# Performance work log

Measured on AMD Instinct MI355X. Metric: run time of the kernel, lower is better.

## Reference

```python
import jax, jax.numpy as jnp
import numpy as np

T, B, IN, H, OUT, L = 2048, 16, 72, 256, 90, 2


def setup_inputs() -> dict:
    key = jax.random.key(0)
    ks = jax.random.split(key, 12)
    s = 0.05
    x = jax.random.normal(ks[0], (T, B, IN), jnp.float32)
    lengths = jnp.clip(jax.random.randint(ks[1], (B,), 1, T + 1), 1, T)
    W1 = jax.random.normal(ks[2], (H, IN), jnp.float32) * s
    b1 = jax.random.normal(ks[3], (H,), jnp.float32) * s
    Wih = jax.random.normal(ks[4], (L, 4 * H, H), jnp.float32) * s
    Whh = jax.random.normal(ks[5], (L, 4 * H, H), jnp.float32) * s
    bih = jax.random.normal(ks[6], (L, 4 * H), jnp.float32) * s
    bhh = jax.random.normal(ks[7], (L, 4 * H), jnp.float32) * s
    W2 = jax.random.normal(ks[8], (OUT, H), jnp.float32) * s
    b2 = jax.random.normal(ks[9], (OUT,), jnp.float32) * s
    return dict(x=x, lengths=lengths, W1=W1, b1=b1, Wih=Wih, Whh=Whh,
                bih=bih, bhh=bhh, W2=W2, b2=b2)


def _lstm_layer(x, mask, Wih, Whh, bih, bhh):
    # x: [T,B,H], mask: [T,B] bool (True = valid frame)
    Hh = Whh.shape[1]
    Bsz = x.shape[1]
    # input projection for all timesteps at once (the only big GEMM)
    gi = jnp.einsum('tbi,gi->tbg', x, Wih) + bih  # [T,B,4H]

    def step(carry, inp):
        h, c = carry
        g_in, m = inp
        g = g_in + h @ Whh.T + bhh
        i, f, gg, o = jnp.split(g, 4, axis=-1)  # PyTorch gate order i,f,g,o
        c_new = jax.nn.sigmoid(f) * c + jax.nn.sigmoid(i) * jnp.tanh(gg)
        h_new = jax.nn.sigmoid(o) * jnp.tanh(c_new)
        m2 = m[:, None]
        # pack semantics: state frozen past each sequence's length, output zero
        h = jnp.where(m2, h_new, h)
        c = jnp.where(m2, c_new, c)
        return (h, c), jnp.where(m2, h_new, jnp.zeros_like(h_new))

    init = (jnp.zeros((Bsz, Hh), x.dtype), jnp.zeros((Bsz, Hh), x.dtype))
    _, ys = jax.lax.scan(step, init, (gi, mask))
    return ys


def reference(x, lengths, W1, b1, Wih, Whh, bih, bhh, W2, b2):
    # linear1 + relu (dropout=0 -> identity)
    h = jax.nn.relu(jnp.einsum('tbi,hi->tbh', x, W1) + b1)
    mask = jnp.arange(T)[:, None] < lengths[None, :]  # [T,B]
    for l in range(L):
        h = _lstm_layer(h, mask, Wih[l], Whh[l], bih[l], bhh[l])
    y = jnp.einsum('tbh,oh->tbo', h, W2) + b2
    # zero out padded frames (they are discarded by the per-sequence slicing)
    return jnp.where(mask[:, :, None], y, jnp.zeros_like(y))
```

## Files before the change

### kernel.cpp

```cpp
#include <hip/hip_runtime.h>
#include <hip/hip_bf16.h>

#define T_STEPS 2048
#define HID 256
#define INF 72
#define OUTF 90
#define HSTR 528

typedef __attribute__((ext_vector_type(4))) float f32x4;
typedef __attribute__((ext_vector_type(8))) short s16x8;

__device__ __forceinline__ unsigned short f2bf(float f) {
  union { float f; unsigned u; } v; v.f = f;
  unsigned r = (v.u + 0x7FFFu + ((v.u >> 16) & 1u)) >> 16;
  return (unsigned short)r;
}
__device__ __forceinline__ float bf2f(unsigned short s) {
  union { unsigned u; float f; } v; v.u = ((unsigned)s) << 16;
  return v.f;
}
__device__ __forceinline__ float sigm(float x) {
  return __builtin_amdgcn_rcpf(1.f + __builtin_amdgcn_exp2f(-1.44269504f * x));
}
__device__ __forceinline__ float tanh_f(float x) {
  return 1.f - 2.f * __builtin_amdgcn_rcpf(1.f + __builtin_amdgcn_exp2f(2.88539008f * x));
}

__global__ __launch_bounds__(256) void inproj(const float* __restrict__ x,
                                              const float* __restrict__ W1,
                                              const float* __restrict__ b1,
                                              float* __restrict__ h0) {
  __shared__ float w1s[HID][INF + 1];
  __shared__ float xs[16][INF];
  const int tid = threadIdx.x;
  const int r0 = blockIdx.x * 16;
  for (int i = tid; i < HID * INF; i += 256) w1s[i / INF][i % INF] = W1[i];
  for (int i = tid; i < 16 * INF; i += 256)
    xs[i / INF][i % INF] = x[(size_t)(r0 + i / INF) * INF + (i % INF)];
  __syncthreads();
  const float bj = b1[tid];
  for (int r = 0; r < 16; ++r) {
    float acc = bj;
#pragma unroll 8
    for (int k = 0; k < INF; ++k) acc += xs[r][k] * w1s[tid][k];
    h0[(size_t)(r0 + r) * HID + tid] = fmaxf(acc, 0.f);
  }
}

__global__ __launch_bounds__(256) void wpack(const float* __restrict__ w,
                                             unsigned short* __restrict__ o) {
  const size_t i = ((size_t)blockIdx.x * 256 + threadIdx.x) * 8;
  f32x4 a = *(const f32x4*)(w + i);
  f32x4 b = *(const f32x4*)(w + i + 4);
  s16x8 v;
#pragma unroll
  for (int e = 0; e < 4; ++e) { v[e] = (short)f2bf(a[e]); v[4 + e] = (short)f2bf(b[e]); }
  *(s16x8*)(o + i) = v;
}

__global__ __launch_bounds__(256) void gi_mfma(const float* __restrict__ h,
                                               const unsigned short* __restrict__ wb,
                                               const float* __restrict__ bih,
                                               const float* __restrict__ bhh,
                                               unsigned short* __restrict__ gi) {
  __shared__ __align__(16) char hs[16 * HSTR];
  __shared__ float bs[1024];
  const int tid = threadIdx.x;
  const int t = blockIdx.x;
  const int lane = tid & 63;
  const int wg = tid >> 6;
  const int j = lane & 15;
  const int hi = lane >> 4;
  for (int i = tid; i < 1024; i += 256) bs[i] = bih[i] + bhh[i];
  {
    const int row = tid >> 4;
    const int c0 = (tid & 15) * 16;
    const float* src = h + ((size_t)t * 16 + row) * 256 + c0;
    f32x4 v0 = *(const f32x4*)(src);
    f32x4 v1 = *(const f32x4*)(src + 4);
    f32x4 v2 = *(const f32x4*)(src + 8);
    f32x4 v3 = *(const f32x4*)(src + 12);
    s16x8 p0, p1;
#pragma unroll
    for (int e = 0; e < 4; ++e) {
      p0[e] = (short)f2bf(v0[e]); p0[4 + e] = (short)f2bf(v1[e]);
      p1[e] = (short)f2bf(v2[e]); p1[4 + e] = (short)f2bf(v3[e]);
    }
    *(s16x8*)(hs + row * HSTR + c0 * 2) = p0;
    *(s16x8*)(hs + row * HSTR + c0 * 2 + 16) = p1;
  }
  __syncthreads();
  const int hread = j * HSTR + hi * 16;
  f32x4 acc[4][4] = {};
#pragma unroll
  for (int kt = 0; kt < 8; ++kt) {
    const int k = kt * 32 + hi * 8;
    const s16x8 a = *(const s16x8*)(hs + hread + kt * 64);
#pragma unroll
    for (int ug2 = 0; ug2 < 4; ++ug2)
#pragma unroll
      for (int q = 0; q < 4; ++q) {
        const s16x8 b = *(const s16x8*)(wb + (((size_t)(q << 8) + wg * 64 + ug2 * 16 + j) << 8) + k);
        acc[ug2][q] = __builtin_amdgcn_mfma_f32_16x16x32_bf16(a, b, acc[ug2][q], 0, 0, 0);
      }
  }
#pragma unroll
  for (int ug2 = 0; ug2 < 4; ++ug2) {
    const int sw = wg * 4 + ug2;
    const int u0 = wg * 64 + ug2 * 16 + j;
    s16x8 o0, o1;
#pragma unroll
    for (int r = 0; r < 4; ++r) {
      o0[r]     = (short)f2bf(acc[ug2][0][r] + bs[u0]);
      o0[4 + r] = (short)f2bf(acc[ug2][1][r] + bs[256 + u0]);
      o1[r]     = (short)f2bf(acc[ug2][2][r] + bs[512 + u0]);
      o1[4 + r] = (short)f2bf(acc[ug2][3][r] + bs[768 + u0]);
    }
    unsigned short* dst = gi + ((size_t)(t * 16 + sw) * 64 + lane) * 16;
    *(s16x8*)(dst) = o0;
    *(s16x8*)(dst + 8) = o1;
  }
}


template <int ROLE>
__device__ __forceinline__ void scan2cu(
    const unsigned short* __restrict__ gi,
    const unsigned short* __restrict__ whbL,
    const int* __restrict__ lengths,
    unsigned short* __restrict__ hb1,
    float* __restrict__ hout,
    unsigned short* hx,
    unsigned* myflag, unsigned* peerflag,
    unsigned* cntA, unsigned* cntB,
    int half)
{
  const int tid  = threadIdx.x;
  const int lane = tid & 63;
  const int w    = tid >> 6;
  const int j    = lane & 15;
  const int hi   = lane >> 4;
  const int u    = half * 128 + w * 16 + j;

  s16x8 wfr[32];
#pragma unroll
  for (int kt = 0; kt < 8; ++kt)
#pragma unroll
    for (int q = 0; q < 4; ++q)
      wfr[kt * 4 + q] =
          *(const s16x8*)(whbL + ((size_t)(q * 256 + u) << 8) + kt * 32 + hi * 8);

  int len[4];
#pragma unroll
  for (int r = 0; r < 4; ++r) len[r] = lengths[hi * 4 + r];
  float c[4] = {};
  unsigned short hprev[4] = {};

  {
    unsigned* z = (unsigned*)hx;
    for (int i = tid; i < 1024; i += 512)
      z[(i >> 6) * 128 + half * 64 + (i & 63)] = 0u;
  }
  asm volatile("s_waitcnt vmcnt(0)" ::: "memory");
  __builtin_amdgcn_s_barrier();
  if (tid == 0) __hip_atomic_store(myflag, 1u, __ATOMIC_RELEASE, __HIP_MEMORY_SCOPE_AGENT);

  unsigned cred = 0;
  if (ROLE == 1) {
    while (cred < 8u) {
      unsigned a = __hip_atomic_load(cntA, __ATOMIC_ACQUIRE, __HIP_MEMORY_SCOPE_AGENT);
      unsigned b = __hip_atomic_load(cntB, __ATOMIC_ACQUIRE, __HIP_MEMORY_SCOPE_AGENT);
      cred = a < b ? a : b;
      if (cred < 8u) __builtin_amdgcn_s_sleep(2);
    }
  }
  const unsigned short* gp = gi + ((size_t)(half * 8 + w) * 64 + lane) * 16;
  s16x8 gE0 = *(const s16x8*)(gp);
  s16x8 gE1 = *(const s16x8*)(gp + 8);
  s16x8 gO0 = *(const s16x8*)(gp + 16384);
  s16x8 gO1 = *(const s16x8*)(gp + 16384 + 8);

  for (int tg = 0; tg < T_STEPS; tg += 4) {
    if (ROLE == 1) {
      const unsigned target = (tg + 8 <= T_STEPS) ? (unsigned)(tg + 8) : (unsigned)T_STEPS;
      while (cred < target) {
        unsigned a = __hip_atomic_load(cntA, __ATOMIC_ACQUIRE, __HIP_MEMORY_SCOPE_AGENT);
        unsigned b = __hip_atomic_load(cntB, __ATOMIC_ACQUIRE, __HIP_MEMORY_SCOPE_AGENT);
        cred = a < b ? a : b;
        if (cred < target) __builtin_amdgcn_s_sleep(2);
      }
    }
#pragma unroll
    for (int ts = 0; ts < 4; ++ts) {
      const int t = tg + ts;
      s16x8& g0 = (ts & 1) ? gO0 : gE0;
      s16x8& g1 = (ts & 1) ? gO1 : gE1;

      while (__hip_atomic_load(peerflag, __ATOMIC_ACQUIRE, __HIP_MEMORY_SCOPE_AGENT) < (unsigned)(t + 1))
        __builtin_amdgcn_s_sleep(1);

      const unsigned short* hsrc = hx + (size_t)(t & 3) * 4096 + j * 256 + hi * 8;
      s16x8 av[8];
#pragma unroll
      for (int kt = 0; kt < 8; ++kt) av[kt] = *(const s16x8*)(hsrc + kt * 32);

      f32x4 acc[4];
#pragma unroll
      for (int r = 0; r < 4; ++r) {
        acc[0][r] = bf2f((unsigned short)g0[r]);
        acc[1][r] = bf2f((unsigned short)g0[4 + r]);
        acc[2][r] = bf2f((unsigned short)g1[r]);
        acc[3][r] = bf2f((unsigned short)g1[4 + r]);
      }
      {
        const int tn = (t + 2 < T_STEPS) ? t + 2 : T_STEPS - 1;
        const unsigned short* gn = gp + (size_t)tn * 16384;
        g0 = *(const s16x8*)(gn);
        g1 = *(const s16x8*)(gn + 8);
      }
#pragma unroll
      for (int kt = 0; kt < 8; ++kt)
#pragma unroll
        for (int q = 0; q < 4; ++q)
          acc[q] = __builtin_amdgcn_mfma_f32_16x16x32_bf16(av[kt], wfr[kt * 4 + q], acc[q], 0, 0, 0);

      unsigned short* hdst = hx + (size_t)((t + 1) & 3) * 4096;
#pragma unroll
      for (int r = 0; r < 4; ++r) {
        const float i_  = sigm(acc[0][r]);
        const float f_  = sigm(acc[1][r]);
        const float tg_ = tanh_f(acc[2][r]);
        const float o_  = sigm(acc[3][r]);
        const float cn = f_ * c[r] + i_ * tg_;
        const float hv = o_ * tanh_f(cn);
        const bool m = t < len[r];
        c[r] = m ? cn : c[r];
        const unsigned short hb = m ? f2bf(hv) : hprev[r];
        hprev[r] = hb;
        const int b = hi * 4 + r;
        hdst[b * 256 + u] = hb;
        if (ROLE == 0) hb1[(size_t)t * 4096 + b * 256 + u] = m ? hb : (unsigned short)0;
        else           hout[((size_t)t * 16 + b) * 256 + u] = m ? hv : 0.f;
      }
      asm volatile("s_waitcnt vmcnt(0)" ::: "memory");
      __builtin_amdgcn_s_barrier();
      if (tid == 0)
        __hip_atomic_store(myflag, (unsigned)(t + 2), __ATOMIC_RELEASE, __HIP_MEMORY_SCOPE_AGENT);
      asm volatile("" ::: "memory");
    }
  }
}

__device__ __forceinline__ void gi2b(int qbase,
    const unsigned short* __restrict__ hb1,
    const unsigned short* __restrict__ wb2,
    const float* __restrict__ bih2, const float* __restrict__ bhh2,
    unsigned short* __restrict__ gf2,
    unsigned* f1a, unsigned* f1b, unsigned* cnt_out)
{
  const int tid = threadIdx.x;
  const int lane = tid & 63;
  const int w = tid >> 6;
  const int j = lane & 15;
  const int hi = lane >> 4;

  s16x8 wfr[2][2][8];
  float bsum[2][2];
#pragma unroll
  for (int qh = 0; qh < 2; ++qh)
#pragma unroll
    for (int ug = 0; ug < 2; ++ug) {
      const int col = (qbase + qh) * 256 + w * 32 + ug * 16 + j;
      bsum[qh][ug] = bih2[col] + bhh2[col];
#pragma unroll
      for (int kt = 0; kt < 8; ++kt)
        wfr[qh][ug][kt] = *(const s16x8*)(wb2 + ((size_t)col << 8) + kt * 32 + hi * 8);
    }

  const int qoff = qbase * 4;
  unsigned cred = 0;
  for (int tg = 0; tg < T_STEPS; tg += 4) {
    const unsigned target = (unsigned)(tg + 5);
    while (cred < target) {
      unsigned a = __hip_atomic_load(f1a, __ATOMIC_ACQUIRE, __HIP_MEMORY_SCOPE_AGENT);
      unsigned b = __hip_atomic_load(f1b, __ATOMIC_ACQUIRE, __HIP_MEMORY_SCOPE_AGENT);
      cred = a < b ? a : b;
      if (cred < target) __builtin_amdgcn_s_sleep(2);
    }
#pragma unroll
    for (int ts = 0; ts < 4; ++ts) {
      const int t = tg + ts;
      const unsigned short* ab = hb1 + (size_t)t * 4096 + j * 256 + hi * 8;
      f32x4 acc[2][2];
#pragma unroll
      for (int qh = 0; qh < 2; ++qh)
#pragma unroll
        for (int ug = 0; ug < 2; ++ug)
#pragma unroll
          for (int r = 0; r < 4; ++r) acc[qh][ug][r] = bsum[qh][ug];
#pragma unroll
      for (int kt = 0; kt < 8; ++kt) {
        const s16x8 a = *(const s16x8*)(ab + kt * 32);
#pragma unroll
        for (int qh = 0; qh < 2; ++qh)
#pragma unroll
          for (int ug = 0; ug < 2; ++ug)
            acc[qh][ug] = __builtin_amdgcn_mfma_f32_16x16x32_bf16(a, wfr[qh][ug][kt], acc[qh][ug], 0, 0, 0);
      }
#pragma unroll
      for (int ug = 0; ug < 2; ++ug) {
        s16x8 o;
#pragma unroll
        for (int r = 0; r < 4; ++r) {
          o[r]     = (short)f2bf(acc[0][ug][r]);
          o[4 + r] = (short)f2bf(acc[1][ug][r]);
        }
        *(s16x8*)(gf2 + ((size_t)(t * 16 + w * 2 + ug) * 64 + lane) * 16 + qoff) = o;
      }
    }
    asm volatile("s_waitcnt vmcnt(0)" ::: "memory");
    __builtin_amdgcn_s_barrier();
    if (tid == 0)
      __hip_atomic_store(cnt_out, (unsigned)(tg + 4), __ATOMIC_RELEASE, __HIP_MEMORY_SCOPE_AGENT);
    asm volatile("" ::: "memory");
  }
}

__global__ __launch_bounds__(512, 2) void fused_pipe(
    const unsigned short* __restrict__ gf1,
    const unsigned short* __restrict__ whb,
    const unsigned short* __restrict__ wb,
    const float* __restrict__ bih, const float* __restrict__ bhh,
    const int* __restrict__ lengths,
    unsigned short* hb1, unsigned short* gf2, float* hout2,
    unsigned short* hx1, unsigned short* hx2, unsigned* sync)
{
  const int bid = blockIdx.x;
  if (bid == 0)
    scan2cu<0>(gf1, whb, lengths, hb1, nullptr, hx1, sync + 0, sync + 32, nullptr, nullptr, 0);
  else if (bid == 8)
    scan2cu<0>(gf1, whb, lengths, hb1, nullptr, hx1, sync + 32, sync + 0, nullptr, nullptr, 1);
  else if (bid == 1)
    scan2cu<1>(gf2, whb + 262144, lengths, nullptr, hout2, hx2, sync + 64, sync + 96, sync + 128, sync + 160, 0);
  else if (bid == 9)
    scan2cu<1>(gf2, whb + 262144, lengths, nullptr, hout2, hx2, sync + 96, sync + 64, sync + 128, sync + 160, 1);
  else if (bid == 2)
    gi2b(0, hb1, wb + 262144, bih + 1024, bhh + 1024, gf2, sync + 0, sync + 32, sync + 128);
  else if (bid == 10)
    gi2b(2, hb1, wb + 262144, bih + 1024, bhh + 1024, gf2, sync + 0, sync + 32, sync + 160);
}

__global__ __launch_bounds__(256) void outproj(const float* __restrict__ h2,
                                               const float* __restrict__ W2,
                                               const float* __restrict__ b2,
                                               const int* __restrict__ lengths,
                                               float* __restrict__ y) {
  __shared__ float w2s[OUTF][HID + 1];
  __shared__ float hs[8][HID + 1];
  const int tid = threadIdx.x;
  const int r0 = blockIdx.x * 8;
  for (int i = tid; i < OUTF * HID; i += 256) w2s[i / HID][i % HID] = W2[i];
  for (int i = tid; i < 8 * HID; i += 256)
    hs[i / HID][i % HID] = h2[(size_t)(r0 + i / HID) * HID + (i % HID)];
  __syncthreads();
  for (int oi = tid; oi < 8 * OUTF; oi += 256) {
    const int r = oi / OUTF, o = oi % OUTF;
    const int row = r0 + r, t = row >> 4, b = row & 15;
    float acc = b2[o];
#pragma unroll 8
    for (int k = 0; k < HID; ++k) acc += hs[r][k] * w2s[o][k];
    y[(size_t)row * OUTF + o] = (t < lengths[b]) ? acc : 0.f;
  }
}

extern "C" void kernel_launch(void* const* d_in, const int* in_sizes, int n_in,
                              void* d_out, int out_size, void* d_ws, size_t ws_size,
                              hipStream_t stream) {
  const float* x      = (const float*)d_in[0];
  const int*   lengths= (const int*)d_in[1];
  const float* W1     = (const float*)d_in[2];
  const float* b1     = (const float*)d_in[3];
  const float* Wih    = (const float*)d_in[4];
  const float* Whh    = (const float*)d_in[5];
  const float* bih    = (const float*)d_in[6];
  const float* bhh    = (const float*)d_in[7];
  const float* W2     = (const float*)d_in[8];
  const float* b2     = (const float*)d_in[9];
  float* out = (float*)d_out;

  char* ws = (char*)d_ws;
  float*          h0   = (float*)(ws);
  unsigned short* gf1  = (unsigned short*)(ws + 33554432);
  unsigned short* hb1  = (unsigned short*)(ws + 100663296);
  unsigned short* gf2  = (unsigned short*)(ws + 117440512);
  float*          h2o  = (float*)(ws + 184549376);
  unsigned short* wb   = (unsigned short*)(ws + 218103808);
  unsigned short* whb  = (unsigned short*)(ws + 219152384);
  unsigned short* hx1  = (unsigned short*)(ws + 220200960);
  unsigned short* hx2  = (unsigned short*)(ws + 220233728);
  unsigned*       sync = (unsigned*)(ws + 220266496);

  wpack<<<256, 256, 0, stream>>>(Wih, wb);
  wpack<<<256, 256, 0, stream>>>(Whh, whb);
  inproj<<<2048, 256, 0, stream>>>(x, W1, b1, h0);
  gi_mfma<<<2048, 256, 0, stream>>>(h0, wb, bih, bhh, gf1);

  hipMemsetAsync((void*)sync, 0, 768, stream);
  fused_pipe<<<11, 512, 0, stream>>>(gf1, whb, wb, bih, bhh, lengths,
                                     hb1, gf2, h2o, hx1, hx2, sync);

  outproj<<<4096, 256, 0, stream>>>(h2o, W2, b2, lengths, out);
}
```

Measured before the change: 10.66 ms.

## Replace per-step block barriers with per-wave flags and transposed MFMA layout

The recurrent scan drops the workgroup barrier and single release flag per timestep. Instead each wave publishes its own relaxed flag, and consumers poll all 16 wave flags with 64-bit loads. The MFMA operands are swapped so each lane holds four consecutive hidden units of one batch. That lets h and outputs be written as packed 64-bit stores and lengths be read once per lane. The gi2b producer is reorganised to compute all four gates per wave. The goal is to cut barrier and cross-CU synchronisation latency on the serial critical path, relying on relaxed atomics plus vmcnt waits for ordering.

```diff
diff --git a/kernel.cpp b/kernel.cpp
--- a/kernel.cpp
+++ b/kernel.cpp
@@ -9,6 +9,7 @@
 
 typedef __attribute__((ext_vector_type(4))) float f32x4;
 typedef __attribute__((ext_vector_type(8))) short s16x8;
+typedef unsigned long long u64;
 
 __device__ __forceinline__ unsigned short f2bf(float f) {
   union { float f; unsigned u; } v; v.f = f;
@@ -24,6 +25,38 @@
 }
 __device__ __forceinline__ float tanh_f(float x) {
   return 1.f - 2.f * __builtin_amdgcn_rcpf(1.f + __builtin_amdgcn_exp2f(2.88539008f * x));
+}
+
+__device__ __forceinline__ u64 ld64(const u64* p) {
+  return __hip_atomic_load(p, __ATOMIC_RELAXED, __HIP_MEMORY_SCOPE_AGENT);
+}
+__device__ __forceinline__ void st64(u64* p, u64 v) {
+  __hip_atomic_store(p, v, __ATOMIC_RELAXED, __HIP_MEMORY_SCOPE_AGENT);
+}
+__device__ __forceinline__ void stflag(unsigned* p, unsigned v) {
+  __hip_atomic_store(p, v, __ATOMIC_RELAXED, __HIP_MEMORY_SCOPE_AGENT);
+}
+__device__ __forceinline__ void wait16(const unsigned* flags, unsigned target) {
+  const u64* fl = (const u64*)flags;
+  unsigned mn;
+  do {
+    mn = 0xFFFFFFFFu;
+#pragma unroll
+    for (int i = 0; i < 8; ++i) {
+      u64 v = ld64(fl + i);
+      unsigned a = (unsigned)v, b = (unsigned)(v >> 32);
+      mn = a < mn ? a : mn;
+      mn = b < mn ? b : mn;
+    }
+    if (mn < target) __builtin_amdgcn_s_sleep(1);
+  } while (mn < target);
+}
+__device__ __forceinline__ void ld_gi(const unsigned short* p, s16x8& a, s16x8& b) {
+  const u64* q = (const u64*)p;
+  union { u64 u[2]; s16x8 v; } x, y;
+  x.u[0] = ld64(q + 0); x.u[1] = ld64(q + 1);
+  y.u[0] = ld64(q + 2); y.u[1] = ld64(q + 3);
+  a = x.v; b = y.v;
 }
 
 __global__ __launch_bounds__(256) void inproj(const float* __restrict__ x,
@@ -100,21 +133,21 @@
     for (int ug2 = 0; ug2 < 4; ++ug2)
 #pragma unroll
       for (int q = 0; q < 4; ++q) {
-        const s16x8 b = *(const s16x8*)(wb + (((size_t)(q << 8) + wg * 64 + ug2 * 16 + j) << 8) + k);
-        acc[ug2][q] = __builtin_amdgcn_mfma_f32_16x16x32_bf16(a, b, acc[ug2][q], 0, 0, 0);
+        const s16x8 bw = *(const s16x8*)(wb + (((size_t)(q << 8) + wg * 64 + ug2 * 16 + j) << 8) + k);
+        acc[ug2][q] = __builtin_amdgcn_mfma_f32_16x16x32_bf16(bw, a, acc[ug2][q], 0, 0, 0);
       }
   }
 #pragma unroll
   for (int ug2 = 0; ug2 < 4; ++ug2) {
     const int sw = wg * 4 + ug2;
-    const int u0 = wg * 64 + ug2 * 16 + j;
+    const int uT = sw * 16 + hi * 4;
     s16x8 o0, o1;
 #pragma unroll
     for (int r = 0; r < 4; ++r) {
-      o0[r]     = (short)f2bf(acc[ug2][0][r] + bs[u0]);
-      o0[4 + r] = (short)f2bf(acc[ug2][1][r] + bs[256 + u0]);
-      o1[r]     = (short)f2bf(acc[ug2][2][r] + bs[512 + u0]);
-      o1[4 + r] = (short)f2bf(acc[ug2][3][r] + bs[768 + u0]);
+      o0[r]     = (short)f2bf(acc[ug2][0][r] + bs[uT + r]);
+      o0[4 + r] = (short)f2bf(acc[ug2][1][r] + bs[256 + uT + r]);
+      o1[r]     = (short)f2bf(acc[ug2][2][r] + bs[512 + uT + r]);
+      o1[4 + r] = (short)f2bf(acc[ug2][3][r] + bs[768 + uT + r]);
     }
     unsigned short* dst = gi + ((size_t)(t * 16 + sw) * 64 + lane) * 16;
     *(s16x8*)(dst) = o0;
@@ -131,8 +164,8 @@
     unsigned short* __restrict__ hb1,
     float* __restrict__ hout,
     unsigned short* hx,
-    unsigned* myflag, unsigned* peerflag,
-    unsigned* cntA, unsigned* cntB,
+    unsigned* flags,
+    unsigned* creds,
     int half)
 {
   const int tid  = threadIdx.x;
@@ -140,7 +173,8 @@
   const int w    = tid >> 6;
   const int j    = lane & 15;
   const int hi   = lane >> 4;
-  const int u    = half * 128 + w * 16 + j;
+  const int uB   = half * 128 + w * 16;
+  const int myf  = half * 8 + w;
 
   s16x8 wfr[32];
 #pragma unroll
@@ -148,44 +182,35 @@
 #pragma unroll
     for (int q = 0; q < 4; ++q)
       wfr[kt * 4 + q] =
-          *(const s16x8*)(whbL + ((size_t)(q * 256 + u) << 8) + kt * 32 + hi * 8);
-
-  int len[4];
-#pragma unroll
-  for (int r = 0; r < 4; ++r) len[r] = lengths[hi * 4 + r];
+          *(const s16x8*)(whbL + ((size_t)(q * 256 + uB + j) << 8) + kt * 32 + hi * 8);
+
+  const int len = lengths[j];
   float c[4] = {};
   unsigned short hprev[4] = {};
 
-  {
-    unsigned* z = (unsigned*)hx;
-    for (int i = tid; i < 1024; i += 512)
-      z[(i >> 6) * 128 + half * 64 + (i & 63)] = 0u;
-  }
-  asm volatile("s_waitcnt vmcnt(0)" ::: "memory");
-  __builtin_amdgcn_s_barrier();
-  if (tid == 0) __hip_atomic_store(myflag, 1u, __ATOMIC_RELEASE, __HIP_MEMORY_SCOPE_AGENT);
+  const unsigned short* gp = gi + ((size_t)(half * 8 + w) * 64 + lane) * 16;
 
   unsigned cred = 0;
   if (ROLE == 1) {
+    const u64* cp = (const u64*)creds;
     while (cred < 8u) {
-      unsigned a = __hip_atomic_load(cntA, __ATOMIC_ACQUIRE, __HIP_MEMORY_SCOPE_AGENT);
-      unsigned b = __hip_atomic_load(cntB, __ATOMIC_ACQUIRE, __HIP_MEMORY_SCOPE_AGENT);
+      u64 v = ld64(cp);
+      unsigned a = (unsigned)v, b = (unsigned)(v >> 32);
       cred = a < b ? a : b;
       if (cred < 8u) __builtin_amdgcn_s_sleep(2);
     }
   }
-  const unsigned short* gp = gi + ((size_t)(half * 8 + w) * 64 + lane) * 16;
-  s16x8 gE0 = *(const s16x8*)(gp);
-  s16x8 gE1 = *(const s16x8*)(gp + 8);
-  s16x8 gO0 = *(const s16x8*)(gp + 16384);
-  s16x8 gO1 = *(const s16x8*)(gp + 16384 + 8);
+  s16x8 gE0, gE1, gO0, gO1;
+  ld_gi(gp, gE0, gE1);
+  ld_gi(gp + 16384, gO0, gO1);
 
   for (int tg = 0; tg < T_STEPS; tg += 4) {
     if (ROLE == 1) {
       const unsigned target = (tg + 8 <= T_STEPS) ? (unsigned)(tg + 8) : (unsigned)T_STEPS;
+      const u64* cp = (const u64*)creds;
       while (cred < target) {
-        unsigned a = __hip_atomic_load(cntA, __ATOMIC_ACQUIRE, __HIP_MEMORY_SCOPE_AGENT);
-        unsigned b = __hip_atomic_load(cntB, __ATOMIC_ACQUIRE, __HIP_MEMORY_SCOPE_AGENT);
+        u64 v = ld64(cp);
+        unsigned a = (unsigned)v, b = (unsigned)(v >> 32);
         cred = a < b ? a : b;
         if (cred < target) __builtin_amdgcn_s_sleep(2);
       }
@@ -196,13 +221,17 @@
       s16x8& g0 = (ts & 1) ? gO0 : gE0;
       s16x8& g1 = (ts & 1) ? gO1 : gE1;
 
-      while (__hip_atomic_load(peerflag, __ATOMIC_ACQUIRE, __HIP_MEMORY_SCOPE_AGENT) < (unsigned)(t + 1))
-        __builtin_amdgcn_s_sleep(1);
-
-      const unsigned short* hsrc = hx + (size_t)(t & 3) * 4096 + j * 256 + hi * 8;
+      wait16(flags, (unsigned)t);
+
+      const u64* hsrc = (const u64*)(hx + (size_t)(t & 3) * 4096 + j * 256) + hi * 2;
       s16x8 av[8];
 #pragma unroll
-      for (int kt = 0; kt < 8; ++kt) av[kt] = *(const s16x8*)(hsrc + kt * 32);
+      for (int kt = 0; kt < 8; ++kt) {
+        union { u64 u[2]; s16x8 v; } x;
+        x.u[0] = ld64(hsrc + kt * 8);
+        x.u[1] = ld64(hsrc + kt * 8 + 1);
+        av[kt] = x.v;
+      }
 
       f32x4 acc[4];
 #pragma unroll
@@ -214,17 +243,17 @@
       }
       {
         const int tn = (t + 2 < T_STEPS) ? t + 2 : T_STEPS - 1;
-        const unsigned short* gn = gp + (size_t)tn * 16384;
-        g0 = *(const s16x8*)(gn);
-        g1 = *(const s16x8*)(gn + 8);
+        ld_gi(gp + (size_t)tn * 16384, g0, g1);
       }
 #pragma unroll
       for (int kt = 0; kt < 8; ++kt)
 #pragma unroll
         for (int q = 0; q < 4; ++q)
-          acc[q] = __builtin_amdgcn_mfma_f32_16x16x32_bf16(av[kt], wfr[kt * 4 + q], acc[q], 0, 0, 0);
-
-      unsigned short* hdst = hx + (size_t)((t + 1) & 3) * 4096;
+          acc[q] = __builtin_amdgcn_mfma_f32_16x16x32_bf16(wfr[kt * 4 + q], av[kt], acc[q], 0, 0, 0);
+
+      u64 hpk = 0, ypk = 0;
+      f32x4 yv;
+      const bool m = t < len;
 #pragma unroll
       for (int r = 0; r < 4; ++r) {
         const float i_  = sigm(acc[0][r]);
@@ -233,96 +262,96 @@
         const float o_  = sigm(acc[3][r]);
         const float cn = f_ * c[r] + i_ * tg_;
         const float hv = o_ * tanh_f(cn);
-        const bool m = t < len[r];
         c[r] = m ? cn : c[r];
         const unsigned short hb = m ? f2bf(hv) : hprev[r];
         hprev[r] = hb;
-        const int b = hi * 4 + r;
-        hdst[b * 256 + u] = hb;
-        if (ROLE == 0) hb1[(size_t)t * 4096 + b * 256 + u] = m ? hb : (unsigned short)0;
-        else           hout[((size_t)t * 16 + b) * 256 + u] = m ? hv : 0.f;
-      }
+        hpk |= (u64)hb << (16 * r);
+        if (ROLE == 0) ypk |= (u64)(m ? hb : (unsigned short)0) << (16 * r);
+        else           yv[r] = m ? hv : 0.f;
+      }
+      st64((u64*)hx + ((((t + 1) & 3) * 4096 + j * 256 + uB + hi * 4) >> 2), hpk);
+      if (ROLE == 0)
+        st64((u64*)hb1 + (((size_t)t * 4096 + j * 256 + uB + hi * 4) >> 2), ypk);
+      else
+        *(f32x4*)(hout + ((size_t)t * 16 + j) * 256 + uB + hi * 4) = yv;
       asm volatile("s_waitcnt vmcnt(0)" ::: "memory");
-      __builtin_amdgcn_s_barrier();
-      if (tid == 0)
-        __hip_atomic_store(myflag, (unsigned)(t + 2), __ATOMIC_RELEASE, __HIP_MEMORY_SCOPE_AGENT);
-      asm volatile("" ::: "memory");
-    }
-  }
-}
-
-__device__ __forceinline__ void gi2b(int qbase,
+      if (lane == 0) stflag(flags + myf, (unsigned)(t + 1));
+    }
+  }
+}
+
+__device__ __forceinline__ void gi2b(int cu,
     const unsigned short* __restrict__ hb1,
     const unsigned short* __restrict__ wb2,
     const float* __restrict__ bih2, const float* __restrict__ bhh2,
     unsigned short* __restrict__ gf2,
-    unsigned* f1a, unsigned* f1b, unsigned* cnt_out)
+    unsigned* flags1, unsigned* cred)
 {
   const int tid = threadIdx.x;
   const int lane = tid & 63;
   const int w = tid >> 6;
   const int j = lane & 15;
   const int hi = lane >> 4;
-
-  s16x8 wfr[2][2][8];
-  float bsum[2][2];
-#pragma unroll
-  for (int qh = 0; qh < 2; ++qh)
-#pragma unroll
-    for (int ug = 0; ug < 2; ++ug) {
-      const int col = (qbase + qh) * 256 + w * 32 + ug * 16 + j;
-      bsum[qh][ug] = bih2[col] + bhh2[col];
-#pragma unroll
-      for (int kt = 0; kt < 8; ++kt)
-        wfr[qh][ug][kt] = *(const s16x8*)(wb2 + ((size_t)col << 8) + kt * 32 + hi * 8);
-    }
-
-  const int qoff = qbase * 4;
-  unsigned cred = 0;
+  const int sw = cu * 8 + w;
+
+  s16x8 wfr[32];
+  float bsum[4][4];
+#pragma unroll
+  for (int kt = 0; kt < 8; ++kt)
+#pragma unroll
+    for (int q = 0; q < 4; ++q)
+      wfr[kt * 4 + q] =
+          *(const s16x8*)(wb2 + ((size_t)(q * 256 + sw * 16 + j) << 8) + kt * 32 + hi * 8);
+#pragma unroll
+  for (int q = 0; q < 4; ++q)
+#pragma unroll
+    for (int r = 0; r < 4; ++r) {
+      const int col = q * 256 + sw * 16 + hi * 4 + r;
+      bsum[q][r] = bih2[col] + bhh2[col];
+    }
+
   for (int tg = 0; tg < T_STEPS; tg += 4) {
-    const unsigned target = (unsigned)(tg + 5);
-    while (cred < target) {
-      unsigned a = __hip_atomic_load(f1a, __ATOMIC_ACQUIRE, __HIP_MEMORY_SCOPE_AGENT);
-      unsigned b = __hip_atomic_load(f1b, __ATOMIC_ACQUIRE, __HIP_MEMORY_SCOPE_AGENT);
-      cred = a < b ? a : b;
-      if (cred < target) __builtin_amdgcn_s_sleep(2);
-    }
+    wait16(flags1, (unsigned)(tg + 4));
 #pragma unroll
     for (int ts = 0; ts < 4; ++ts) {
       const int t = tg + ts;
-      const unsigned short* ab = hb1 + (size_t)t * 4096 + j * 256 + hi * 8;
-      f32x4 acc[2][2];
-#pragma unroll
-      for (int qh = 0; qh < 2; ++qh)
-#pragma unroll
-        for (int ug = 0; ug < 2; ++ug)
-#pragma unroll
-          for (int r = 0; r < 4; ++r) acc[qh][ug][r] = bsum[qh][ug];
+      const u64* ab = (const u64*)(hb1 + (size_t)t * 4096 + j * 256) + hi * 2;
+      s16x8 av[8];
 #pragma unroll
       for (int kt = 0; kt < 8; ++kt) {
-        const s16x8 a = *(const s16x8*)(ab + kt * 32);
-#pragma unroll
-        for (int qh = 0; qh < 2; ++qh)
-#pragma unroll
-          for (int ug = 0; ug < 2; ++ug)
-            acc[qh][ug] = __builtin_amdgcn_mfma_f32_16x16x32_bf16(a, wfr[qh][ug][kt], acc[qh][ug], 0, 0, 0);
-      }
-#pragma unroll
-      for (int ug = 0; ug < 2; ++ug) {
-        s16x8 o;
-#pragma unroll
-        for (int r = 0; r < 4; ++r) {
-          o[r]     = (short)f2bf(acc[0][ug][r]);
-          o[4 + r] = (short)f2bf(acc[1][ug][r]);
-        }
-        *(s16x8*)(gf2 + ((size_t)(t * 16 + w * 2 + ug) * 64 + lane) * 16 + qoff) = o;
-      }
+        union { u64 u[2]; s16x8 v; } x;
+        x.u[0] = ld64(ab + kt * 8);
+        x.u[1] = ld64(ab + kt * 8 + 1);
+        av[kt] = x.v;
+      }
+      f32x4 acc[4];
+#pragma unroll
+      for (int q = 0; q < 4; ++q)
+#pragma unroll
+        for (int r = 0; r < 4; ++r) acc[q][r] = bsum[q][r];
+#pragma unroll
+      for (int kt = 0; kt < 8; ++kt)
+#pragma unroll
+        for (int q = 0; q < 4; ++q)
+          acc[q] = __builtin_amdgcn_mfma_f32_16x16x32_bf16(wfr[kt * 4 + q], av[kt], acc[q], 0, 0, 0);
+      u64 p0 = 0, p1 = 0;
+#pragma unroll
+      for (int r = 0; r < 4; ++r) {
+        p0 |= (u64)f2bf(acc[0][r]) << (16 * r);
+        p1 |= (u64)f2bf(acc[2][r]) << (16 * r);
+      }
+      u64 q0 = 0, q1 = 0;
+#pragma unroll
+      for (int r = 0; r < 4; ++r) {
+        q0 |= (u64)f2bf(acc[1][r]) << (16 * r);
+        q1 |= (u64)f2bf(acc[3][r]) << (16 * r);
+      }
+      u64* dst = (u64*)gf2 + ((size_t)(t * 16 + sw) * 64 + lane) * 4;
+      st64(dst, p0); st64(dst + 1, q0); st64(dst + 2, p1); st64(dst + 3, q1);
     }
     asm volatile("s_waitcnt vmcnt(0)" ::: "memory");
     __builtin_amdgcn_s_barrier();
-    if (tid == 0)
-      __hip_atomic_store(cnt_out, (unsigned)(tg + 4), __ATOMIC_RELEASE, __HIP_MEMORY_SCOPE_AGENT);
-    asm volatile("" ::: "memory");
+    if (tid == 0) stflag(cred, (unsigned)(tg + 4));
   }
 }
 
@@ -337,17 +366,17 @@
 {
   const int bid = blockIdx.x;
   if (bid == 0)
-    scan2cu<0>(gf1, whb, lengths, hb1, nullptr, hx1, sync + 0, sync + 32, nullptr, nullptr, 0);
+    scan2cu<0>(gf1, whb, lengths, hb1, nullptr, hx1, sync, nullptr, 0);
   else if (bid == 8)
-    scan2cu<0>(gf1, whb, lengths, hb1, nullptr, hx1, sync + 32, sync + 0, nullptr, nullptr, 1);
+    scan2cu<0>(gf1, whb, lengths, hb1, nullptr, hx1, sync, nullptr, 1);
   else if (bid == 1)
-    scan2cu<1>(gf2, whb + 262144, lengths, nullptr, hout2, hx2, sync + 64, sync + 96, sync + 128, sync + 160, 0);
+    scan2cu<1>(gf2, whb + 262144, lengths, nullptr, hout2, hx2, sync + 16, sync + 32, 0);
   else if (bid == 9)
-    scan2cu<1>(gf2, whb + 262144, lengths, nullptr, hout2, hx2, sync + 96, sync + 64, sync + 128, sync + 160, 1);
+    scan2cu<1>(gf2, whb + 262144, lengths, nullptr, hout2, hx2, sync + 16, sync + 32, 1);
   else if (bid == 2)
-    gi2b(0, hb1, wb + 262144, bih + 1024, bhh + 1024, gf2, sync + 0, sync + 32, sync + 128);
+    gi2b(0, hb1, wb + 262144, bih + 1024, bhh + 1024, gf2, sync, sync + 32);
   else if (bid == 10)
-    gi2b(2, hb1, wb + 262144, bih + 1024, bhh + 1024, gf2, sync + 0, sync + 32, sync + 160);
+    gi2b(1, hb1, wb + 262144, bih + 1024, bhh + 1024, gf2, sync, sync + 33);
 }
 
 __global__ __launch_bounds__(256) void outproj(const float* __restrict__ h2,
@@ -405,7 +434,7 @@
   inproj<<<2048, 256, 0, stream>>>(x, W1, b1, h0);
   gi_mfma<<<2048, 256, 0, stream>>>(h0, wb, bih, bhh, gf1);
 
-  hipMemsetAsync((void*)sync, 0, 768, stream);
+  hipMemsetAsync((void*)hx1, 0, 2 * 32768 + 1024, stream);
   fused_pipe<<<11, 512, 0, stream>>>(gf1, whb, wb, bih, bhh, lengths,
                                      hb1, gf2, h2o, hx1, hx2, sync);
 
```

Result: slower. 23.96 ms (+124.7%).
